# Kernel optimization log

Hardware: AMD Instinct MI355X
Metric: run time of the kernel (lower is better)

Reference implementation:

```python
import jax, jax.numpy as jnp
import numpy as np

N = 50000
NEG_SLOPE = 0.2  # PyG GATConv default negative_slope


def _gat_layer(x, src, dst, edge_attr, W, We, a_src, a_dst, a_edge, bias):
    """Single-head PyG GATConv (heads=1, concat=True, add_self_loops=True,
    fill_value='mean' for self-loop edge_attr, dropout inactive / eval mode)."""
    n = x.shape[0]
    # add self loops; self-loop edge_attr = per-feature mean of edge_attr
    loop = jnp.arange(n)
    src2 = jnp.concatenate([src, loop])
    dst2 = jnp.concatenate([dst, loop])
    ea_loop = jnp.broadcast_to(edge_attr.mean(axis=0, keepdims=True), (n, edge_attr.shape[1]))
    ea = jnp.concatenate([edge_attr, ea_loop], axis=0)          # [E', edge_dim]

    h = x @ W                                                    # [N, C_out]
    a_s = h @ a_src                                              # [N]
    a_d = h @ a_dst                                              # [N]
    a_e = (ea @ We) @ a_edge                                     # [E']

    alpha = jax.nn.leaky_relu(a_s[src2] + a_d[dst2] + a_e, NEG_SLOPE)  # [E']
    # segment softmax over incoming edges of each dst node
    amax = jax.ops.segment_max(alpha, dst2, num_segments=n)     # [N]
    ex = jnp.exp(alpha - amax[dst2])                             # [E']
    denom = jax.ops.segment_sum(ex, dst2, num_segments=n)       # [N]
    w = ex / denom[dst2]                                         # [E']

    msg = h[src2] * w[:, None]                                   # [E', C_out]
    out = jax.ops.segment_sum(msg, dst2, num_segments=n) + bias  # [N, C_out]
    return out


def setup_inputs() -> dict:
    key = jax.random.key(0)
    ks = jax.random.split(key, 16)
    E, C_in, C_h, C_out, Ed = 800000, 128, 256, 128, 8
    s = 0.05
    inp = {
        "x": jax.random.normal(ks[0], (N, C_in), dtype=jnp.float32),
        "edge_index": jax.random.randint(ks[1], (2, E), 0, N, dtype=jnp.int32),
        "edge_attr": jax.random.normal(ks[2], (E, Ed), dtype=jnp.float32),
        # layer 1 params
        "W1": jax.random.normal(ks[3], (C_in, C_h), dtype=jnp.float32) * s,
        "We1": jax.random.normal(ks[4], (Ed, C_h), dtype=jnp.float32) * s,
        "as1": jax.random.normal(ks[5], (C_h,), dtype=jnp.float32) * s,
        "ad1": jax.random.normal(ks[6], (C_h,), dtype=jnp.float32) * s,
        "ae1": jax.random.normal(ks[7], (C_h,), dtype=jnp.float32) * s,
        "b1": jnp.zeros((C_h,), dtype=jnp.float32),
        # layer 2 params
        "W2": jax.random.normal(ks[8], (C_h, C_out), dtype=jnp.float32) * s,
        "We2": jax.random.normal(ks[9], (Ed, C_out), dtype=jnp.float32) * s,
        "as2": jax.random.normal(ks[10], (C_out,), dtype=jnp.float32) * s,
        "ad2": jax.random.normal(ks[11], (C_out,), dtype=jnp.float32) * s,
        "ae2": jax.random.normal(ks[12], (C_out,), dtype=jnp.float32) * s,
        "b2": jnp.zeros((C_out,), dtype=jnp.float32),
    }
    return inp


def reference(x, edge_index, edge_attr, W1, We1, as1, ad1, ae1, b1,
              W2, We2, as2, ad2, ae2, b2):
    src, dst = edge_index[0], edge_index[1]
    h = _gat_layer(x, src, dst, edge_attr, W1, We1, as1, ad1, ae1, b1)
    h = jax.nn.relu(h)  # relu between layers, not after last
    out = _gat_layer(h, src, dst, edge_attr, W2, We2, as2, ad2, ae2, b2)
    return out
```

## Files before the change

### kernel.cpp

```cpp
#include <hip/hip_runtime.h>
#include <hip/hip_bf16.h>


#define NEG_SLOPE 0.2f
#define EHB 1024

typedef unsigned short u16;
typedef short short8 __attribute__((ext_vector_type(8)));
typedef float v4f __attribute__((ext_vector_type(4)));
typedef u16 u16x4 __attribute__((ext_vector_type(4)));
typedef u16 u16x8 __attribute__((ext_vector_type(8)));

__device__ __forceinline__ u16 f2bf(float f) {
    unsigned u = __float_as_uint(f);
    return (u16)((u + 0x7fffu + ((u >> 16) & 1u)) >> 16);
}
__device__ __forceinline__ float bf2f(u16 h) {
    return __uint_as_float(((unsigned)h) << 16);
}
__device__ __forceinline__ float bf_lo(int v) { return __uint_as_float(((unsigned)v) << 16); }
__device__ __forceinline__ float bf_hi(int v) { return __uint_as_float(((unsigned)v) & 0xffff0000u); }
__device__ __forceinline__ float lrelu(float x) {
    return x >= 0.f ? x : NEG_SLOPE * x;
}
__device__ __forceinline__ int ld_acq(int* p) {
    return __hip_atomic_load(p, __ATOMIC_ACQUIRE, __HIP_MEMORY_SCOPE_AGENT);
}
__device__ __forceinline__ void st_rel(int* p, int v) {
    __hip_atomic_store(p, v, __ATOMIC_RELEASE, __HIP_MEMORY_SCOPE_AGENT);
}

__global__ __launch_bounds__(256) void pre_fat_kernel(
        const float* __restrict__ ea, const int* __restrict__ dst,
        const float* __restrict__ We1, const float* __restrict__ ae1v,
        const float* __restrict__ We2, const float* __restrict__ ae2v,
        float* __restrict__ mean_acc, int* __restrict__ deg,
        float2* __restrict__ aEe, int E,
        const float* __restrict__ W1, u16* __restrict__ w1thi, u16* __restrict__ w1tlo,
        const float* __restrict__ W2, u16* __restrict__ w2thi, u16* __restrict__ w2tlo,
        float* __restrict__ we_vec1g, float* __restrict__ we_vec2g) {
    int tid = threadIdx.x;
    if (blockIdx.x >= EHB) {
        int t = (blockIdx.x - EHB) * 256 + tid;
        if (t < 128 * 256) {
            int k = t >> 8, m = t & 255;
            float v = W1[t];
            u16 h = f2bf(v);
            w1thi[(size_t)m * 128 + k] = h;
            w1tlo[(size_t)m * 128 + k] = f2bf(v - bf2f(h));
        } else {
            t -= 128 * 256;
            int k = t >> 7, m = t & 127;
            float v = W2[t];
            u16 h = f2bf(v);
            w2thi[(size_t)m * 256 + k] = h;
            w2tlo[(size_t)m * 256 + k] = f2bf(v - bf2f(h));
        }
        return;
    }
    __shared__ float red[8];
    __shared__ float wv[16];
    if (tid < 16) { wv[tid] = 0.f; if (tid < 8) red[tid] = 0.f; }
    __syncthreads();
    {
        float a1 = ae1v[tid];
        int lane = tid & 63;
#pragma unroll
        for (int j = 0; j < 8; ++j) {
            float v = We1[j * 256 + tid] * a1;
#pragma unroll
            for (int o = 32; o; o >>= 1) v += __shfl_down(v, o);
            if (lane == 0) atomicAdd(&wv[j], v);
        }
        if (tid < 128) {
            float a2 = ae2v[tid];
#pragma unroll
            for (int j = 0; j < 8; ++j) {
                float v = We2[j * 128 + tid] * a2;
#pragma unroll
                for (int o = 32; o; o >>= 1) v += __shfl_down(v, o);
                if (lane == 0) atomicAdd(&wv[8 + j], v);
            }
        }
    }
    __syncthreads();
    if (blockIdx.x == 0 && tid < 16) {
        if (tid < 8) we_vec1g[tid] = wv[tid];
        else         we_vec2g[tid - 8] = wv[tid];
    }
    float s[8] = {0.f};
    int stride = EHB * 256;
    for (int e = blockIdx.x * 256 + tid; e < E; e += stride) {
        atomicAdd(&deg[dst[e]], 1);
        const float4 v0 = *(const float4*)&ea[(size_t)e * 8];
        const float4 v1 = *(const float4*)&ea[(size_t)e * 8 + 4];
        s[0] += v0.x; s[1] += v0.y; s[2] += v0.z; s[3] += v0.w;
        s[4] += v1.x; s[5] += v1.y; s[6] += v1.z; s[7] += v1.w;
        float s1 = v0.x * wv[0] + v0.y * wv[1] + v0.z * wv[2] + v0.w * wv[3]
                 + v1.x * wv[4] + v1.y * wv[5] + v1.z * wv[6] + v1.w * wv[7];
        float s2 = v0.x * wv[8] + v0.y * wv[9] + v0.z * wv[10] + v0.w * wv[11]
                 + v1.x * wv[12] + v1.y * wv[13] + v1.z * wv[14] + v1.w * wv[15];
        aEe[e] = make_float2(s1, s2);
    }
#pragma unroll
    for (int j = 0; j < 8; ++j) atomicAdd(&red[j], s[j]);
    __syncthreads();
    if (tid < 8) atomicAdd(&mean_acc[tid], red[tid]);
}

__global__ __launch_bounds__(256) void scan_fused_kernel(
        const int* __restrict__ deg, int* __restrict__ row_start,
        int* __restrict__ cursor, int* __restrict__ partials, int* __restrict__ pprefix,
        int* __restrict__ gcount, int* __restrict__ gflag, int N, int n,
        const float* __restrict__ mean_acc, float Einv,
        const float* __restrict__ we_vec1, const float* __restrict__ we_vec2,
        float* __restrict__ ae_loop) {
    __shared__ int s[256];
    __shared__ int amLast, bprefix;
    int t = threadIdx.x, bid = blockIdx.x;
    int i = bid * 256 + t;
    int v = (i < N) ? deg[i] : 0;
    s[t] = v; __syncthreads();
    for (int off = 1; off < 256; off <<= 1) {
        int u = (t >= off) ? s[t - off] : 0;
        __syncthreads();
        s[t] += u;
        __syncthreads();
    }
    int incl = s[t];
    int total = s[255];
    if (t == 0) {
        partials[bid] = total;
        __threadfence();
        int c = __hip_atomic_fetch_add(gcount, 1, __ATOMIC_ACQ_REL, __HIP_MEMORY_SCOPE_AGENT);
        amLast = (c == (int)gridDim.x - 1);
    }
    __syncthreads();
    if (amLast) {
        int G = gridDim.x;
        int pv = (t < G) ? ld_acq(&partials[t]) : 0;
        __syncthreads();
        s[t] = pv; __syncthreads();
        for (int off = 1; off < 256; off <<= 1) {
            int u = (t >= off) ? s[t - off] : 0;
            __syncthreads();
            s[t] += u;
            __syncthreads();
        }
        if (t < G) pprefix[t] = s[t] - pv;
        if (t == 0) {
            float s1 = 0.f, s2 = 0.f;
#pragma unroll
            for (int j = 0; j < 8; ++j) {
                float m = mean_acc[j] * Einv;
                s1 += m * we_vec1[j];
                s2 += m * we_vec2[j];
            }
            ae_loop[0] = s1; ae_loop[1] = s2;
        }
        __threadfence();
        __syncthreads();
        if (t == 0) st_rel(gflag, 1);
    }
    if (t == 0) {
        while (ld_acq(gflag) == 0) __builtin_amdgcn_s_sleep(2);
        bprefix = ld_acq(&pprefix[bid]);
    }
    __syncthreads();
    int ex = bprefix + incl - v;
    if (i < n) row_start[i] = ex;
    if (i < N) cursor[i] = ex;
}

#define BK 32
#define LDA 40
__global__ __launch_bounds__(256) void gemm1_fill_fat_kernel(
        const float* __restrict__ A32,
        const u16* __restrict__ Bh_g, const u16* __restrict__ Bl_g,
        u16* __restrict__ Cb, int Nrows, int K, int M,
        const float* __restrict__ av, const float* __restrict__ bv,
        float* __restrict__ as_out, float* __restrict__ ad_out, int Gg, int gx,
        const int* __restrict__ src, const int* __restrict__ dst,
        const float2* __restrict__ aEe, int* __restrict__ cursor,
        float4* __restrict__ epack, int E) {
    __shared__ u16 Ah[128 * LDA], Bh[128 * LDA], Bl[128 * LDA];
    int tid = threadIdx.x;
    if ((int)blockIdx.x >= Gg) {
        int e = ((int)blockIdx.x - Gg) * 256 + tid;
        if (e < E) {
            int d = dst[e];
            int idx = atomicAdd(&cursor[d], 1);
            float2 a = aEe[e];
            epack[idx] = make_float4(__int_as_float(src[e]), a.x, a.y, 0.f);
        }
        return;
    }
    int lane = tid & 63;
    int wv = tid >> 6;
    int wm = wv >> 1, wn = wv & 1;
    int l15 = lane & 15, quad = lane >> 4;
    int rb = ((int)blockIdx.x / gx) * 128;
    int cb = ((int)blockIdx.x % gx) * 128;

    v4f acc[4][4];
#pragma unroll
    for (int mi = 0; mi < 4; ++mi)
#pragma unroll
        for (int ni = 0; ni < 4; ++ni) acc[mi][ni] = (v4f){0.f, 0.f, 0.f, 0.f};

    int sr = tid >> 1;
    int sc = (tid & 1) * 16;

    for (int kc = 0; kc < K; kc += BK) {
        int gr = rb + sr;
        u16x8 a0 = {0,0,0,0,0,0,0,0}, a1 = {0,0,0,0,0,0,0,0};
        if (gr < Nrows) {
            const float* pa = A32 + (size_t)gr * K + kc + sc;
            float4 f0 = *(const float4*)pa;
            float4 f1 = *(const float4*)(pa + 4);
            float4 f2 = *(const float4*)(pa + 8);
            float4 f3 = *(const float4*)(pa + 12);
            a0 = (u16x8){f2bf(f0.x), f2bf(f0.y), f2bf(f0.z), f2bf(f0.w),
                         f2bf(f1.x), f2bf(f1.y), f2bf(f1.z), f2bf(f1.w)};
            a1 = (u16x8){f2bf(f2.x), f2bf(f2.y), f2bf(f2.z), f2bf(f2.w),
                         f2bf(f3.x), f2bf(f3.y), f2bf(f3.z), f2bf(f3.w)};
        }
        size_t bb = (size_t)(cb + sr) * K + kc + sc;
        u16x8 b0 = *(const u16x8*)(Bh_g + bb);
        u16x8 b1 = *(const u16x8*)(Bh_g + bb + 8);
        u16x8 b2 = *(const u16x8*)(Bl_g + bb);
        u16x8 b3 = *(const u16x8*)(Bl_g + bb + 8);
        *(u16x8*)&Ah[sr * LDA + sc] = a0;
        *(u16x8*)&Ah[sr * LDA + sc + 8] = a1;
        *(u16x8*)&Bh[sr * LDA + sc] = b0;
        *(u16x8*)&Bh[sr * LDA + sc + 8] = b1;
        *(u16x8*)&Bl[sr * LDA + sc] = b2;
        *(u16x8*)&Bl[sr * LDA + sc + 8] = b3;
        __syncthreads();
        short8 ah[4], bh[4], bl[4];
#pragma unroll
        for (int mi = 0; mi < 4; ++mi)
            ah[mi] = *(const short8*)&Ah[(wm * 64 + mi * 16 + l15) * LDA + quad * 8];
#pragma unroll
        for (int ni = 0; ni < 4; ++ni) {
            int r = (wn * 64 + ni * 16 + l15) * LDA + quad * 8;
            bh[ni] = *(const short8*)&Bh[r];
            bl[ni] = *(const short8*)&Bl[r];
        }
#pragma unroll
        for (int mi = 0; mi < 4; ++mi)
#pragma unroll
            for (int ni = 0; ni < 4; ++ni) {
                acc[mi][ni] = __builtin_amdgcn_mfma_f32_16x16x32_bf16(ah[mi], bh[ni], acc[mi][ni], 0, 0, 0);
                acc[mi][ni] = __builtin_amdgcn_mfma_f32_16x16x32_bf16(ah[mi], bl[ni], acc[mi][ni], 0, 0, 0);
            }
        __syncthreads();
    }
#pragma unroll
    for (int mi = 0; mi < 4; ++mi)
#pragma unroll
        for (int ni = 0; ni < 4; ++ni)
#pragma unroll
            for (int reg = 0; reg < 4; ++reg) {
                int row = rb + wm * 64 + mi * 16 + quad * 4 + reg;
                if (row < Nrows)
                    Cb[(size_t)row * M + cb + wn * 64 + ni * 16 + l15] = f2bf(acc[mi][ni][reg]);
            }
    float sd[4][4] = {}, dd[4][4] = {};
#pragma unroll
    for (int ni = 0; ni < 4; ++ni) {
        int col = cb + wn * 64 + ni * 16 + l15;
        float a = av[col], b = bv[col];
#pragma unroll
        for (int mi = 0; mi < 4; ++mi)
#pragma unroll
            for (int reg = 0; reg < 4; ++reg) {
                sd[mi][reg] += acc[mi][ni][reg] * a;
                dd[mi][reg] += acc[mi][ni][reg] * b;
            }
    }
#pragma unroll
    for (int off = 1; off < 16; off <<= 1)
#pragma unroll
        for (int mi = 0; mi < 4; ++mi)
#pragma unroll
            for (int reg = 0; reg < 4; ++reg) {
                sd[mi][reg] += __shfl_xor(sd[mi][reg], off);
                dd[mi][reg] += __shfl_xor(dd[mi][reg], off);
            }
    if (l15 == 0)
#pragma unroll
        for (int mi = 0; mi < 4; ++mi) {
            int row0 = rb + wm * 64 + mi * 16 + quad * 4;
#pragma unroll
            for (int reg = 0; reg < 4; ++reg)
                if (row0 + reg < Nrows) {
                    atomicAdd(as_out + row0 + reg, sd[mi][reg]);
                    atomicAdd(ad_out + row0 + reg, dd[mi][reg]);
                }
        }
}

__global__ __launch_bounds__(256) void gemm_mfma_kernel(
        const u16* __restrict__ A_g,
        const u16* __restrict__ Bh_g, const u16* __restrict__ Bl_g,
        u16* __restrict__ Cb, int Nrows, int K, int M,
        const float* __restrict__ av, const float* __restrict__ bv,
        float* __restrict__ as_out, float* __restrict__ ad_out) {
    __shared__ u16 Ah[128 * LDA], Bh[128 * LDA], Bl[128 * LDA];
    int tid = threadIdx.x;
    int lane = tid & 63;
    int wv = tid >> 6;
    int wm = wv >> 1, wn = wv & 1;
    int l15 = lane & 15, quad = lane >> 4;
    int rb = blockIdx.y * 128;
    int cb = blockIdx.x * 128;

    v4f acc[4][4];
#pragma unroll
    for (int mi = 0; mi < 4; ++mi)
#pragma unroll
        for (int ni = 0; ni < 4; ++ni) acc[mi][ni] = (v4f){0.f, 0.f, 0.f, 0.f};

    int sr = tid >> 1;
    int sc = (tid & 1) * 16;

    for (int kc = 0; kc < K; kc += BK) {
        int gr = rb + sr;
        u16x8 a0 = {0,0,0,0,0,0,0,0}, a1 = {0,0,0,0,0,0,0,0};
        if (gr < Nrows) {
            size_t ba = (size_t)gr * K + kc + sc;
            a0 = *(const u16x8*)(A_g + ba);
            a1 = *(const u16x8*)(A_g + ba + 8);
        }
        size_t bb = (size_t)(cb + sr) * K + kc + sc;
        u16x8 b0 = *(const u16x8*)(Bh_g + bb);
        u16x8 b1 = *(const u16x8*)(Bh_g + bb + 8);
        u16x8 b2 = *(const u16x8*)(Bl_g + bb);
        u16x8 b3 = *(const u16x8*)(Bl_g + bb + 8);
        *(u16x8*)&Ah[sr * LDA + sc] = a0;
        *(u16x8*)&Ah[sr * LDA + sc + 8] = a1;
        *(u16x8*)&Bh[sr * LDA + sc] = b0;
        *(u16x8*)&Bh[sr * LDA + sc + 8] = b1;
        *(u16x8*)&Bl[sr * LDA + sc] = b2;
        *(u16x8*)&Bl[sr * LDA + sc + 8] = b3;
        __syncthreads();
        short8 ah[4], bh[4], bl[4];
#pragma unroll
        for (int mi = 0; mi < 4; ++mi)
            ah[mi] = *(const short8*)&Ah[(wm * 64 + mi * 16 + l15) * LDA + quad * 8];
#pragma unroll
        for (int ni = 0; ni < 4; ++ni) {
            int r = (wn * 64 + ni * 16 + l15) * LDA + quad * 8;
            bh[ni] = *(const short8*)&Bh[r];
            bl[ni] = *(const short8*)&Bl[r];
        }
#pragma unroll
        for (int mi = 0; mi < 4; ++mi)
#pragma unroll
            for (int ni = 0; ni < 4; ++ni) {
                acc[mi][ni] = __builtin_amdgcn_mfma_f32_16x16x32_bf16(ah[mi], bh[ni], acc[mi][ni], 0, 0, 0);
                acc[mi][ni] = __builtin_amdgcn_mfma_f32_16x16x32_bf16(ah[mi], bl[ni], acc[mi][ni], 0, 0, 0);
            }
        __syncthreads();
    }
#pragma unroll
    for (int mi = 0; mi < 4; ++mi)
#pragma unroll
        for (int ni = 0; ni < 4; ++ni)
#pragma unroll
            for (int reg = 0; reg < 4; ++reg) {
                int row = rb + wm * 64 + mi * 16 + quad * 4 + reg;
                if (row < Nrows)
                    Cb[(size_t)row * M + cb + wn * 64 + ni * 16 + l15] = f2bf(acc[mi][ni][reg]);
            }
    float sd[4][4] = {}, dd[4][4] = {};
#pragma unroll
    for (int ni = 0; ni < 4; ++ni) {
        int col = cb + wn * 64 + ni * 16 + l15;
        float a = av[col], b = bv[col];
#pragma unroll
        for (int mi = 0; mi < 4; ++mi)
#pragma unroll
            for (int reg = 0; reg < 4; ++reg) {
                sd[mi][reg] += acc[mi][ni][reg] * a;
                dd[mi][reg] += acc[mi][ni][reg] * b;
            }
    }
#pragma unroll
    for (int off = 1; off < 16; off <<= 1)
#pragma unroll
        for (int mi = 0; mi < 4; ++mi)
#pragma unroll
            for (int reg = 0; reg < 4; ++reg) {
                sd[mi][reg] += __shfl_xor(sd[mi][reg], off);
                dd[mi][reg] += __shfl_xor(dd[mi][reg], off);
            }
    if (l15 == 0)
#pragma unroll
        for (int mi = 0; mi < 4; ++mi) {
            int row0 = rb + wm * 64 + mi * 16 + quad * 4;
#pragma unroll
            for (int reg = 0; reg < 4; ++reg)
                if (row0 + reg < Nrows) {
                    atomicAdd(as_out + row0 + reg, sd[mi][reg]);
                    atomicAdd(ad_out + row0 + reg, dd[mi][reg]);
                }
        }
}

__global__ __launch_bounds__(256) void agg1_kernel(const int* __restrict__ row_start,
                                                   const float4* __restrict__ epack,
                                                   const float* __restrict__ asv,
                                                   const float* __restrict__ adv,
                                                   const float* __restrict__ ae_loop,
                                                   const u16* __restrict__ Hb,
                                                   u16* __restrict__ ohi,
                                                   const float* __restrict__ bias, int N) {
    __shared__ float2 xch[4][64];
    int lane = threadIdx.x & 63;
    int wvi = threadIdx.x >> 6;
    int node = blockIdx.x * 4 + wvi;
    if (node >= N) return;
    int st = row_start[node], en = row_start[node + 1];
    float ad = adv[node];
    float aloop = lrelu(asv[node] + ad + ae_loop[0]);
    float m = aloop, sum = 1.f;
    float acc0, acc1, acc2, acc3;
    {
        int2 hv = *(const int2*)(Hb + (size_t)node * 256 + lane * 4);
        acc0 = bf_lo(hv.x); acc1 = bf_hi(hv.x);
        acc2 = bf_lo(hv.y); acc3 = bf_hi(hv.y);
    }
    for (int base = st; base < en; base += 64) {
        int i = base + lane;
        float al = -3.0e38f; int sreg = 0;
        if (i < en) {
            float4 ep = epack[i];
            sreg = __float_as_int(ep.x);
            al = lrelu(asv[sreg] + ad + ep.y);
        }
        float cm = al;
#pragma unroll
        for (int o = 1; o < 64; o <<= 1) cm = fmaxf(cm, __shfl_xor(cm, o));
        if (cm > m) {
            float sc = __expf(m - cm);
            acc0 *= sc; acc1 *= sc; acc2 *= sc; acc3 *= sc;
            sum *= sc; m = cm;
        }
        float w = (i < en) ? __expf(al - m) : 0.f;
        float wsum = w;
#pragma unroll
        for (int o = 1; o < 64; o <<= 1) wsum += __shfl_xor(wsum, o);
        sum += wsum;
        xch[wvi][lane] = make_float2(w, __int_as_float(sreg));
        int cnt = min(64, en - base);
        int j = 0;
        for (; j + 4 <= cnt; j += 4) {
            float2 e0 = xch[wvi][j], e1 = xch[wvi][j + 1];
            float2 e2 = xch[wvi][j + 2], e3 = xch[wvi][j + 3];
            int2 h0 = *(const int2*)(Hb + (size_t)__float_as_int(e0.y) * 256 + lane * 4);
            int2 h1 = *(const int2*)(Hb + (size_t)__float_as_int(e1.y) * 256 + lane * 4);
            int2 h2 = *(const int2*)(Hb + (size_t)__float_as_int(e2.y) * 256 + lane * 4);
            int2 h3 = *(const int2*)(Hb + (size_t)__float_as_int(e3.y) * 256 + lane * 4);
            acc0 += e0.x * bf_lo(h0.x) + e1.x * bf_lo(h1.x) + e2.x * bf_lo(h2.x) + e3.x * bf_lo(h3.x);
            acc1 += e0.x * bf_hi(h0.x) + e1.x * bf_hi(h1.x) + e2.x * bf_hi(h2.x) + e3.x * bf_hi(h3.x);
            acc2 += e0.x * bf_lo(h0.y) + e1.x * bf_lo(h1.y) + e2.x * bf_lo(h2.y) + e3.x * bf_lo(h3.y);
            acc3 += e0.x * bf_hi(h0.y) + e1.x * bf_hi(h1.y) + e2.x * bf_hi(h2.y) + e3.x * bf_hi(h3.y);
        }
        for (; j < cnt; ++j) {
            float2 e0 = xch[wvi][j];
            int2 h0 = *(const int2*)(Hb + (size_t)__float_as_int(e0.y) * 256 + lane * 4);
            acc0 += e0.x * bf_lo(h0.x); acc1 += e0.x * bf_hi(h0.x);
            acc2 += e0.x * bf_lo(h0.y); acc3 += e0.x * bf_hi(h0.y);
        }
    }
    float inv = 1.f / sum;
    const float4 bvv = *(const float4*)(bias + lane * 4);
    float t0 = acc0 * inv + bvv.x, t1 = acc1 * inv + bvv.y;
    float t2 = acc2 * inv + bvv.z, t3 = acc3 * inv + bvv.w;
    t0 = t0 > 0.f ? t0 : 0.f; t1 = t1 > 0.f ? t1 : 0.f;
    t2 = t2 > 0.f ? t2 : 0.f; t3 = t3 > 0.f ? t3 : 0.f;
    u16x4 h;
    h.x = f2bf(t0); h.y = f2bf(t1); h.z = f2bf(t2); h.w = f2bf(t3);
    *(u16x4*)(ohi + (size_t)node * 256 + lane * 4) = h;
}

__global__ __launch_bounds__(256) void agg2_kernel(const int* __restrict__ row_start,
                                                   const float4* __restrict__ epack,
                                                   const float* __restrict__ asv,
                                                   const float* __restrict__ adv,
                                                   const float* __restrict__ ae_loop,
                                                   const u16* __restrict__ Hb,
                                                   float* __restrict__ out,
                                                   const float* __restrict__ bias, int N) {
    __shared__ float2 xch[4][64];
    int lane = threadIdx.x & 63;
    int wvi = threadIdx.x >> 6;
    int node = blockIdx.x * 4 + wvi;
    if (node >= N) return;
    int st = row_start[node], en = row_start[node + 1];
    float ad = adv[node];
    float aloop = lrelu(asv[node] + ad + ae_loop[1]);
    float m = aloop, sum = 1.f;
    float acc0, acc1;
    {
        int hv = *(const int*)(Hb + (size_t)node * 128 + lane * 2);
        acc0 = bf_lo(hv); acc1 = bf_hi(hv);
    }
    for (int base = st; base < en; base += 64) {
        int i = base + lane;
        float al = -3.0e38f; int sreg = 0;
        if (i < en) {
            float4 ep = epack[i];
            sreg = __float_as_int(ep.x);
            al = lrelu(asv[sreg] + ad + ep.z);
        }
        float cm = al;
#pragma unroll
        for (int o = 1; o < 64; o <<= 1) cm = fmaxf(cm, __shfl_xor(cm, o));
        if (cm > m) {
            float sc = __expf(m - cm);
            acc0 *= sc; acc1 *= sc;
            sum *= sc; m = cm;
        }
        float w = (i < en) ? __expf(al - m) : 0.f;
        float wsum = w;
#pragma unroll
        for (int o = 1; o < 64; o <<= 1) wsum += __shfl_xor(wsum, o);
        sum += wsum;
        xch[wvi][lane] = make_float2(w, __int_as_float(sreg));
        int cnt = min(64, en - base);
        int j = 0;
        for (; j + 4 <= cnt; j += 4) {
            float2 e0 = xch[wvi][j], e1 = xch[wvi][j + 1];
            float2 e2 = xch[wvi][j + 2], e3 = xch[wvi][j + 3];
            int h0 = *(const int*)(Hb + (size_t)__float_as_int(e0.y) * 128 + lane * 2);
            int h1 = *(const int*)(Hb + (size_t)__float_as_int(e1.y) * 128 + lane * 2);
            int h2 = *(const int*)(Hb + (size_t)__float_as_int(e2.y) * 128 + lane * 2);
            int h3 = *(const int*)(Hb + (size_t)__float_as_int(e3.y) * 128 + lane * 2);
            acc0 += e0.x * bf_lo(h0) + e1.x * bf_lo(h1) + e2.x * bf_lo(h2) + e3.x * bf_lo(h3);
            acc1 += e0.x * bf_hi(h0) + e1.x * bf_hi(h1) + e2.x * bf_hi(h2) + e3.x * bf_hi(h3);
        }
        for (; j < cnt; ++j) {
            float2 e0 = xch[wvi][j];
            int h0 = *(const int*)(Hb + (size_t)__float_as_int(e0.y) * 128 + lane * 2);
            acc0 += e0.x * bf_lo(h0); acc1 += e0.x * bf_hi(h0);
        }
    }
    float inv = 1.f / sum;
    size_t o = (size_t)node * 128 + lane * 2;
    out[o]     = acc0 * inv + bias[lane * 2];
    out[o + 1] = acc1 * inv + bias[lane * 2 + 1];
}

extern "C" void kernel_launch(void* const* d_in, const int* in_sizes, int n_in,
                              void* d_out, int out_size, void* d_ws, size_t ws_size,
                              hipStream_t stream) {
    const int Cin = 128, Ch = 256, Co = 128;
    const int N = in_sizes[0] / Cin;
    const int E = in_sizes[1] / 2;

    const float* x   = (const float*)d_in[0];
    const int*   src = (const int*)d_in[1];
    const int*   dst = src + E;
    const float* ea  = (const float*)d_in[2];
    const float* W1  = (const float*)d_in[3];
    const float* We1 = (const float*)d_in[4];
    const float* as1 = (const float*)d_in[5];
    const float* ad1 = (const float*)d_in[6];
    const float* ae1 = (const float*)d_in[7];
    const float* b1  = (const float*)d_in[8];
    const float* W2  = (const float*)d_in[9];
    const float* We2 = (const float*)d_in[10];
    const float* as2 = (const float*)d_in[11];
    const float* ad2 = (const float*)d_in[12];
    const float* ae2 = (const float*)d_in[13];
    const float* b2  = (const float*)d_in[14];
    float* out = (float*)d_out;

    float* ws = (float*)d_ws;
    size_t off = 0;
    u16* h1b = (u16*)(ws + off); off += (size_t)N * Ch / 2;
    u16* g1b = (u16*)(ws + off); off += (size_t)N * Ch / 2;
    float4* epack = (float4*)(ws + off); off += (size_t)E * 4;
    float2* aEe   = (float2*)(ws + off); off += (size_t)E * 2;
    int* row_start = (int*)(ws + off); off += (size_t)N + 1;
    int* cursor    = (int*)(ws + off); off += (size_t)N;
    int* partials  = (int*)(ws + off); off += 256;
    int* pprefix   = (int*)(ws + off); off += 256;
    u16* w1thi = (u16*)(ws + off); off += (size_t)Cin * Ch / 2;
    u16* w1tlo = (u16*)(ws + off); off += (size_t)Cin * Ch / 2;
    u16* w2thi = (u16*)(ws + off); off += (size_t)Ch * Co / 2;
    u16* w2tlo = (u16*)(ws + off); off += (size_t)Ch * Co / 2;
    int*   deg  = (int*)(ws + off); off += (size_t)N + 1;
    float* asv1 = ws + off; off += (size_t)N;
    float* adv1 = ws + off; off += (size_t)N;
    float* asv2 = ws + off; off += (size_t)N;
    float* adv2 = ws + off; off += (size_t)N;
    float* misc = ws + off; off += 32;
    float* mean_acc = misc;
    float* we_vec1  = misc + 8;
    float* we_vec2  = misc + 16;
    float* ae_loop  = misc + 24;
    int* gcount = (int*)(ws + off); off += 1;
    int* gflag  = (int*)(ws + off); off += 1;

    const int n1 = N + 1;
    const int nscan = (n1 + 255) / 256;

    hipMemsetAsync(deg, 0, ((size_t)5 * N + 35) * sizeof(float), stream);

    pre_fat_kernel<<<EHB + 256, 256, 0, stream>>>(
        ea, dst, We1, ae1, We2, ae2, mean_acc, deg, aEe, E,
        W1, w1thi, w1tlo, W2, w2thi, w2tlo, we_vec1, we_vec2);

    scan_fused_kernel<<<nscan, 256, 0, stream>>>(
        deg, row_start, cursor, partials, pprefix, gcount, gflag, N, n1,
        mean_acc, 1.0f / (float)E, we_vec1, we_vec2, ae_loop);

    {
        int gx = Ch / 128;
        int Gg = gx * ((N + 127) / 128);
        int Fb = (E + 255) / 256;
        gemm1_fill_fat_kernel<<<Gg + Fb, 256, 0, stream>>>(
            x, w1thi, w1tlo, h1b, N, Cin, Ch, as1, ad1, asv1, adv1, Gg, gx,
            src, dst, aEe, cursor, epack, E);
    }
    agg1_kernel<<<(N + 3) / 4, 256, 0, stream>>>(row_start, epack, asv1, adv1, ae_loop,
                                                 h1b, g1b, b1, N);

    u16* h2b = h1b;
    {
        dim3 grid(Co / 128, (N + 127) / 128);
        gemm_mfma_kernel<<<grid, 256, 0, stream>>>(g1b, w2thi, w2tlo, h2b, N, Ch, Co,
                                                   as2, ad2, asv2, adv2);
    }
    agg2_kernel<<<(N + 3) / 4, 256, 0, stream>>>(row_start, epack, asv2, adv2, ae_loop,
                                                 h2b, out, b2, N);
}
```

Measured before the change: 406.6 us.

## Move CSR edge fill into scan kernel behind a grid barrier, split gemm1

The edge scatter that fills the CSR-ordered epack array now runs in the scan kernel. It waits behind a second software grid barrier and has each thread handle 8 edges, with their loads, cursor atomics and stores batched to raise memory-level parallelism. gemm1 becomes a plain 2D-grid GEMM with no fill blocks appended. The change drops the fat-kernel mix of GEMM and fill blocks but serialises the fill before the GEMM rather than overlapping them. The grid barrier relies on all scan blocks being co-resident, which holds for about 196 blocks.

```diff
diff --git a/kernel.cpp b/kernel.cpp
--- a/kernel.cpp
+++ b/kernel.cpp
@@ -108,13 +108,16 @@
     if (tid < 8) atomicAdd(&mean_acc[tid], red[tid]);
 }
 
-__global__ __launch_bounds__(256) void scan_fused_kernel(
+__global__ __launch_bounds__(256) void scan_fill_kernel(
         const int* __restrict__ deg, int* __restrict__ row_start,
         int* __restrict__ cursor, int* __restrict__ partials, int* __restrict__ pprefix,
-        int* __restrict__ gcount, int* __restrict__ gflag, int N, int n,
+        int* __restrict__ gcount, int* __restrict__ gflag,
+        int* __restrict__ gcount2, int* __restrict__ gflag2, int N, int n,
         const float* __restrict__ mean_acc, float Einv,
         const float* __restrict__ we_vec1, const float* __restrict__ we_vec2,
-        float* __restrict__ ae_loop) {
+        float* __restrict__ ae_loop,
+        const int* __restrict__ src, const int* __restrict__ dst,
+        const float2* __restrict__ aEe, float4* __restrict__ epack, int E) {
     __shared__ int s[256];
     __shared__ int amLast, bprefix;
     int t = threadIdx.x, bid = blockIdx.x;
@@ -170,37 +173,55 @@
     int ex = bprefix + incl - v;
     if (i < n) row_start[i] = ex;
     if (i < N) cursor[i] = ex;
+
+    __threadfence();
+    __syncthreads();
+    if (t == 0) {
+        int c2 = __hip_atomic_fetch_add(gcount2, 1, __ATOMIC_ACQ_REL, __HIP_MEMORY_SCOPE_AGENT);
+        if (c2 == (int)gridDim.x - 1) st_rel(gflag2, 1);
+        while (ld_acq(gflag2) == 0) __builtin_amdgcn_s_sleep(2);
+    }
+    __syncthreads();
+
+    const int T = (int)gridDim.x * 256;
+    for (int e0 = bid * 256 + t; e0 < E; e0 += 8 * T) {
+        int dv[8], sv[8]; float2 av[8];
+#pragma unroll
+        for (int u = 0; u < 8; ++u) {
+            int e = e0 + u * T;
+            if (e < E) { dv[u] = dst[e]; sv[u] = src[e]; av[u] = aEe[e]; }
+        }
+        int ix[8];
+#pragma unroll
+        for (int u = 0; u < 8; ++u) {
+            int e = e0 + u * T;
+            if (e < E) ix[u] = atomicAdd(&cursor[dv[u]], 1);
+        }
+#pragma unroll
+        for (int u = 0; u < 8; ++u) {
+            int e = e0 + u * T;
+            if (e < E)
+                epack[ix[u]] = make_float4(__int_as_float(sv[u]), av[u].x, av[u].y, 0.f);
+        }
+    }
 }
 
 #define BK 32
 #define LDA 40
-__global__ __launch_bounds__(256) void gemm1_fill_fat_kernel(
+__global__ __launch_bounds__(256) void gemm1_kernel(
         const float* __restrict__ A32,
         const u16* __restrict__ Bh_g, const u16* __restrict__ Bl_g,
         u16* __restrict__ Cb, int Nrows, int K, int M,
         const float* __restrict__ av, const float* __restrict__ bv,
-        float* __restrict__ as_out, float* __restrict__ ad_out, int Gg, int gx,
-        const int* __restrict__ src, const int* __restrict__ dst,
-        const float2* __restrict__ aEe, int* __restrict__ cursor,
-        float4* __restrict__ epack, int E) {
+        float* __restrict__ as_out, float* __restrict__ ad_out) {
     __shared__ u16 Ah[128 * LDA], Bh[128 * LDA], Bl[128 * LDA];
     int tid = threadIdx.x;
-    if ((int)blockIdx.x >= Gg) {
-        int e = ((int)blockIdx.x - Gg) * 256 + tid;
-        if (e < E) {
-            int d = dst[e];
-            int idx = atomicAdd(&cursor[d], 1);
-            float2 a = aEe[e];
-            epack[idx] = make_float4(__int_as_float(src[e]), a.x, a.y, 0.f);
-        }
-        return;
-    }
     int lane = tid & 63;
     int wv = tid >> 6;
     int wm = wv >> 1, wn = wv & 1;
     int l15 = lane & 15, quad = lane >> 4;
-    int rb = ((int)blockIdx.x / gx) * 128;
-    int cb = ((int)blockIdx.x % gx) * 128;
+    int rb = blockIdx.y * 128;
+    int cb = blockIdx.x * 128;
 
     v4f acc[4][4];
 #pragma unroll
@@ -603,29 +624,30 @@
     float* we_vec1  = misc + 8;
     float* we_vec2  = misc + 16;
     float* ae_loop  = misc + 24;
-    int* gcount = (int*)(ws + off); off += 1;
-    int* gflag  = (int*)(ws + off); off += 1;
+    int* gcount  = (int*)(ws + off); off += 1;
+    int* gflag   = (int*)(ws + off); off += 1;
+    int* gcount2 = (int*)(ws + off); off += 1;
+    int* gflag2  = (int*)(ws + off); off += 1;
 
     const int n1 = N + 1;
     const int nscan = (n1 + 255) / 256;
 
-    hipMemsetAsync(deg, 0, ((size_t)5 * N + 35) * sizeof(float), stream);
+    hipMemsetAsync(deg, 0, ((size_t)5 * N + 37) * sizeof(float), stream);
 
     pre_fat_kernel<<<EHB + 256, 256, 0, stream>>>(
         ea, dst, We1, ae1, We2, ae2, mean_acc, deg, aEe, E,
         W1, w1thi, w1tlo, W2, w2thi, w2tlo, we_vec1, we_vec2);
 
-    scan_fused_kernel<<<nscan, 256, 0, stream>>>(
-        deg, row_start, cursor, partials, pprefix, gcount, gflag, N, n1,
-        mean_acc, 1.0f / (float)E, we_vec1, we_vec2, ae_loop);
+    scan_fill_kernel<<<nscan, 256, 0, stream>>>(
+        deg, row_start, cursor, partials, pprefix, gcount, gflag,
+        gcount2, gflag2, N, n1,
+        mean_acc, 1.0f / (float)E, we_vec1, we_vec2, ae_loop,
+        src, dst, aEe, epack, E);
 
     {
-        int gx = Ch / 128;
-        int Gg = gx * ((N + 127) / 128);
-        int Fb = (E + 255) / 256;
-        gemm1_fill_fat_kernel<<<Gg + Fb, 256, 0, stream>>>(
-            x, w1thi, w1tlo, h1b, N, Cin, Ch, as1, ad1, asv1, adv1, Gg, gx,
-            src, dst, aEe, cursor, epack, E);
+        dim3 grid(Ch / 128, (N + 127) / 128);
+        gemm1_kernel<<<grid, 256, 0, stream>>>(x, w1thi, w1tlo, h1b, N, Cin, Ch,
+                                               as1, ad1, asv1, adv1);
     }
     agg1_kernel<<<(N + 3) / 4, 256, 0, stream>>>(row_start, epack, asv1, adv1, ae_loop,
                                                  h1b, g1b, b1, N);
```

New measurement: 430.0 us. 1.06x slower.

## Record per-edge rank in degree count to drop fill atomics; unroll gathers

Applied to the files above, without the earlier changes.

The degree-counting pass now saves the value returned by each atomic increment as that edge's rank within its destination. The CSR fill then computes its slot as row_start plus rank, with no second round of atomics and no cursor array to initialise. EHB is doubled to launch more edge blocks, and both aggregation kernels gain an 8-way unrolled gather loop so more row loads are in flight at once. The cost is an extra E-sized int array that must be written and read back, plus higher register pressure from the unrolling.

```diff
diff --git a/kernel.cpp b/kernel.cpp
--- a/kernel.cpp
+++ b/kernel.cpp
@@ -3,7 +3,7 @@
 
 
 #define NEG_SLOPE 0.2f
-#define EHB 1024
+#define EHB 2048
 
 typedef unsigned short u16;
 typedef short short8 __attribute__((ext_vector_type(8)));
@@ -35,6 +35,7 @@
         const float* __restrict__ We1, const float* __restrict__ ae1v,
         const float* __restrict__ We2, const float* __restrict__ ae2v,
         float* __restrict__ mean_acc, int* __restrict__ deg,
+        int* __restrict__ rank,
         float2* __restrict__ aEe, int E,
         const float* __restrict__ W1, u16* __restrict__ w1thi, u16* __restrict__ w1tlo,
         const float* __restrict__ W2, u16* __restrict__ w2thi, u16* __restrict__ w2tlo,
@@ -91,7 +92,8 @@
     float s[8] = {0.f};
     int stride = EHB * 256;
     for (int e = blockIdx.x * 256 + tid; e < E; e += stride) {
-        atomicAdd(&deg[dst[e]], 1);
+        int d = dst[e];
+        rank[e] = atomicAdd(&deg[d], 1);
         const float4 v0 = *(const float4*)&ea[(size_t)e * 8];
         const float4 v1 = *(const float4*)&ea[(size_t)e * 8 + 4];
         s[0] += v0.x; s[1] += v0.y; s[2] += v0.z; s[3] += v0.w;
@@ -110,7 +112,7 @@
 
 __global__ __launch_bounds__(256) void scan_fused_kernel(
         const int* __restrict__ deg, int* __restrict__ row_start,
-        int* __restrict__ cursor, int* __restrict__ partials, int* __restrict__ pprefix,
+        int* __restrict__ partials, int* __restrict__ pprefix,
         int* __restrict__ gcount, int* __restrict__ gflag, int N, int n,
         const float* __restrict__ mean_acc, float Einv,
         const float* __restrict__ we_vec1, const float* __restrict__ we_vec2,
@@ -169,7 +171,6 @@
     __syncthreads();
     int ex = bprefix + incl - v;
     if (i < n) row_start[i] = ex;
-    if (i < N) cursor[i] = ex;
 }
 
 #define BK 32
@@ -181,7 +182,8 @@
         const float* __restrict__ av, const float* __restrict__ bv,
         float* __restrict__ as_out, float* __restrict__ ad_out, int Gg, int gx,
         const int* __restrict__ src, const int* __restrict__ dst,
-        const float2* __restrict__ aEe, int* __restrict__ cursor,
+        const float2* __restrict__ aEe, const int* __restrict__ row_start,
+        const int* __restrict__ rank,
         float4* __restrict__ epack, int E) {
     __shared__ u16 Ah[128 * LDA], Bh[128 * LDA], Bl[128 * LDA];
     int tid = threadIdx.x;
@@ -189,7 +191,7 @@
         int e = ((int)blockIdx.x - Gg) * 256 + tid;
         if (e < E) {
             int d = dst[e];
-            int idx = atomicAdd(&cursor[d], 1);
+            int idx = row_start[d] + rank[e];
             float2 a = aEe[e];
             epack[idx] = make_float4(__int_as_float(src[e]), a.x, a.y, 0.f);
         }
@@ -456,6 +458,19 @@
         xch[wvi][lane] = make_float2(w, __int_as_float(sreg));
         int cnt = min(64, en - base);
         int j = 0;
+        for (; j + 8 <= cnt; j += 8) {
+            float2 e[8]; int2 h[8];
+#pragma unroll
+            for (int q = 0; q < 8; ++q) e[q] = xch[wvi][j + q];
+#pragma unroll
+            for (int q = 0; q < 8; ++q)
+                h[q] = *(const int2*)(Hb + (size_t)__float_as_int(e[q].y) * 256 + lane * 4);
+#pragma unroll
+            for (int q = 0; q < 8; ++q) {
+                acc0 += e[q].x * bf_lo(h[q].x); acc1 += e[q].x * bf_hi(h[q].x);
+                acc2 += e[q].x * bf_lo(h[q].y); acc3 += e[q].x * bf_hi(h[q].y);
+            }
+        }
         for (; j + 4 <= cnt; j += 4) {
             float2 e0 = xch[wvi][j], e1 = xch[wvi][j + 1];
             float2 e2 = xch[wvi][j + 2], e3 = xch[wvi][j + 3];
@@ -532,6 +547,18 @@
         xch[wvi][lane] = make_float2(w, __int_as_float(sreg));
         int cnt = min(64, en - base);
         int j = 0;
+        for (; j + 8 <= cnt; j += 8) {
+            float2 e[8]; int h[8];
+#pragma unroll
+            for (int q = 0; q < 8; ++q) e[q] = xch[wvi][j + q];
+#pragma unroll
+            for (int q = 0; q < 8; ++q)
+                h[q] = *(const int*)(Hb + (size_t)__float_as_int(e[q].y) * 128 + lane * 2);
+#pragma unroll
+            for (int q = 0; q < 8; ++q) {
+                acc0 += e[q].x * bf_lo(h[q]); acc1 += e[q].x * bf_hi(h[q]);
+            }
+        }
         for (; j + 4 <= cnt; j += 4) {
             float2 e0 = xch[wvi][j], e1 = xch[wvi][j + 1];
             float2 e2 = xch[wvi][j + 2], e3 = xch[wvi][j + 3];
@@ -585,8 +612,8 @@
     u16* g1b = (u16*)(ws + off); off += (size_t)N * Ch / 2;
     float4* epack = (float4*)(ws + off); off += (size_t)E * 4;
     float2* aEe   = (float2*)(ws + off); off += (size_t)E * 2;
+    int* rank     = (int*)(ws + off); off += (size_t)E;
     int* row_start = (int*)(ws + off); off += (size_t)N + 1;
-    int* cursor    = (int*)(ws + off); off += (size_t)N;
     int* partials  = (int*)(ws + off); off += 256;
     int* pprefix   = (int*)(ws + off); off += 256;
     u16* w1thi = (u16*)(ws + off); off += (size_t)Cin * Ch / 2;
@@ -612,11 +639,11 @@
     hipMemsetAsync(deg, 0, ((size_t)5 * N + 35) * sizeof(float), stream);
 
     pre_fat_kernel<<<EHB + 256, 256, 0, stream>>>(
-        ea, dst, We1, ae1, We2, ae2, mean_acc, deg, aEe, E,
+        ea, dst, We1, ae1, We2, ae2, mean_acc, deg, rank, aEe, E,
         W1, w1thi, w1tlo, W2, w2thi, w2tlo, we_vec1, we_vec2);
 
     scan_fused_kernel<<<nscan, 256, 0, stream>>>(
-        deg, row_start, cursor, partials, pprefix, gcount, gflag, N, n1,
+        deg, row_start, partials, pprefix, gcount, gflag, N, n1,
         mean_acc, 1.0f / (float)E, we_vec1, we_vec2, ae_loop);
 
     {
@@ -625,7 +652,7 @@
         int Fb = (E + 255) / 256;
         gemm1_fill_fat_kernel<<<Gg + Fb, 256, 0, stream>>>(
             x, w1thi, w1tlo, h1b, N, Cin, Ch, as1, ad1, asv1, adv1, Gg, gx,
-            src, dst, aEe, cursor, epack, E);
+            src, dst, aEe, row_start, rank, epack, E);
     }
     agg1_kernel<<<(N + 3) / 4, 256, 0, stream>>>(row_start, epack, asv1, adv1, ae_loop,
                                                  h1b, g1b, b1, N);
```

New measurement: 386.8 us. 4.9% less time.
